# Kernel optimization log

Hardware: AMD Instinct MI355X
Metric: run time of the kernel (lower is better)

The kernel has to match this reference:

```python
import jax, jax.numpy as jnp
import numpy as np

HEADS = 8

def setup_inputs() -> dict:
    key = jax.random.key(0)
    ks = jax.random.split(key, 11)
    B, S, E = 4, 2048, 512
    sc = 1.0 / np.sqrt(E)
    return {
        "inputs": jax.random.normal(ks[0], (B, S, E), jnp.float32),
        "entangle": jax.random.uniform(ks[1], (S,), jnp.float32),
        "Wq": jax.random.normal(ks[2], (E, E), jnp.float32) * sc,
        "bq": jax.random.normal(ks[3], (E,), jnp.float32) * 0.01,
        "Wk": jax.random.normal(ks[4], (E, E), jnp.float32) * sc,
        "bk": jax.random.normal(ks[5], (E,), jnp.float32) * 0.01,
        "Wv": jax.random.normal(ks[6], (E, E), jnp.float32) * sc,
        "bv": jax.random.normal(ks[7], (E,), jnp.float32) * 0.01,
        "Wo": jax.random.normal(ks[8], (E, E), jnp.float32) * sc,
        "bo": jax.random.normal(ks[9], (E,), jnp.float32) * 0.01,
    }

def reference(inputs, entangle, Wq, bq, Wk, bk, Wv, bv, Wo, bo):
    B, S, E = inputs.shape
    H = HEADS
    D = E // H
    # torch nn.Linear: y = x @ W.T + b
    Q = (inputs @ Wq.T + bq).reshape(B, S, H, D)
    K = (inputs @ Wk.T + bk).reshape(B, S, H, D)
    V = (inputs @ Wv.T + bv).reshape(B, S, H, D)
    scores = jnp.einsum('bqhd,bkhd->bhqk', Q, K) / jnp.sqrt(jnp.float32(D))
    # entangle broadcast as (1,1,S,1): per-query-position scaling before softmax
    scores = scores * entangle[None, None, :, None]
    attn = jax.nn.softmax(scores, axis=-1)
    out = jnp.einsum('bhqk,bkhd->bqhd', attn, V).reshape(B, S, E)
    return out @ Wo.T + bo
```

## Files before the change

### kernel.cpp

```cpp
#include <hip/hip_runtime.h>
#include <hip/hip_bf16.h>

#define BB 4
#define SS 2048
#define EE 512
#define HH 8
#define DD 64

typedef __attribute__((ext_vector_type(8))) short bf16x8;
typedef __attribute__((ext_vector_type(4))) float f32x4;
typedef __attribute__((ext_vector_type(4))) unsigned int u32x4;

__device__ __forceinline__ unsigned short f2bf(float f) {
    __hip_bfloat16 h = __float2bfloat16(f);
    return *reinterpret_cast<unsigned short*>(&h);
}

__device__ __forceinline__ unsigned int cvtpk(float lo, float hi) {
    unsigned int r;
    asm("v_cvt_pk_bf16_f32 %0, %1, %2" : "=v"(r) : "v"(lo), "v"(hi));
    return r;
}

__device__ __forceinline__ void pl32(unsigned int& a, unsigned int& b) {
    asm("v_permlane32_swap_b32 %0, %1" : "+v"(a), "+v"(b));
}
__device__ __forceinline__ void pl16(unsigned int& a, unsigned int& b) {
    asm("v_permlane16_swap_b32 %0, %1" : "+v"(a), "+v"(b));
}

__device__ __forceinline__ void gll16(const unsigned short* g, unsigned short* l) {
    __builtin_amdgcn_global_load_lds(
        (const __attribute__((address_space(1))) unsigned int*)g,
        (__attribute__((address_space(3))) unsigned int*)l,
        16, 0, 0);
}

__global__ __launch_bounds__(256)
void cast_all(const float* __restrict__ x,
              const float* __restrict__ wq, const float* __restrict__ wk,
              const float* __restrict__ wv, const float* __restrict__ wo,
              unsigned short* __restrict__ xb,
              unsigned short* __restrict__ wqb, unsigned short* __restrict__ wkb,
              unsigned short* __restrict__ wvb, unsigned short* __restrict__ wob)
{
    const int bid = blockIdx.x;
    const float* src; unsigned short* dst; int lb;
    if (bid < 4096)      { src = x;  dst = xb;  lb = bid; }
    else {
        const int t = (bid - 4096) >> 8;
        lb = (bid - 4096) & 255;
        switch (t) {
            case 0:  src = wq; dst = wqb; break;
            case 1:  src = wk; dst = wkb; break;
            case 2:  src = wv; dst = wvb; break;
            default: src = wo; dst = wob; break;
        }
    }
    const int i = lb * 256 + threadIdx.x;
    const float4 v = reinterpret_cast<const float4*>(src)[i];
    ushort4 o;
    o.x = f2bf(v.x); o.y = f2bf(v.y); o.z = f2bf(v.z); o.w = f2bf(v.w);
    reinterpret_cast<ushort4*>(dst)[i] = o;
}

template<typename OutT, bool TRANSPOSE_V, int TM>
__global__ __launch_bounds__(256)
void gemm_mfma_nt(const unsigned short* __restrict__ A,
                  const unsigned short* __restrict__ W0, const float* __restrict__ b0, OutT* __restrict__ C0,
                  const unsigned short* __restrict__ W1, const float* __restrict__ b1, OutT* __restrict__ C1,
                  const unsigned short* __restrict__ W2, const float* __restrict__ b2, OutT* __restrict__ C2,
                  const float* __restrict__ rowscale,
                  int M, int N, int K)
{
    const unsigned short* W = (blockIdx.z == 0) ? W0 : (blockIdx.z == 1) ? W1 : W2;
    const float* bias       = (blockIdx.z == 0) ? b0 : (blockIdx.z == 1) ? b1 : b2;
    OutT* C                 = (blockIdx.z == 0) ? C0 : (blockIdx.z == 1) ? C1 : C2;

    constexpr int MT = TM / 32;
    __shared__ unsigned short As[2][TM * 32];
    __shared__ unsigned short Bs[2][128 * 32];

    const int tid  = threadIdx.x;
    const int wave = tid >> 6, lane = tid & 63;
    const int quad = lane >> 4, r16 = lane & 15;
    const int m0 = blockIdx.x * TM, n0 = blockIdx.y * 128;
    const int wm0 = (wave >> 1) * (TM / 2), wn0 = (wave & 1) * 64;

    f32x4 acc[MT][4];
    const f32x4 zero = {0.f, 0.f, 0.f, 0.f};
    #pragma unroll
    for (int i = 0; i < MT; ++i)
        #pragma unroll
        for (int j = 0; j < 4; ++j) acc[i][j] = zero;

    const int swz = (r16 >> 1) & 3;

    auto stage = [&](int bi, int k0) {
        #pragma unroll
        for (int j = 0; j < TM / 64; ++j) {
            const int cb = wave * 64 + j * 256;
            const int c  = cb + lane;
            const int row = c >> 2, cc = (c & 3) ^ ((row >> 1) & 3);
            gll16(&A[(size_t)(m0 + row) * K + k0 + cc * 8], &As[bi][cb * 8]);
        }
        #pragma unroll
        for (int j = 0; j < 2; ++j) {
            const int cb = wave * 64 + j * 256;
            const int c  = cb + lane;
            const int row = c >> 2, cc = (c & 3) ^ ((row >> 1) & 3);
            gll16(&W[(size_t)(n0 + row) * K + k0 + cc * 8], &Bs[bi][cb * 8]);
        }
    };

    stage(0, 0);

    const int NI = K / 32;
    for (int i = 0; i < NI; ++i) {
        const int cur = i & 1;
        __syncthreads();
        if (i + 1 < NI) stage(cur ^ 1, (i + 1) * 32);

        bf16x8 af[MT], bfr[4];
        #pragma unroll
        for (int t = 0; t < MT; ++t)
            af[t]  = *reinterpret_cast<bf16x8*>(&As[cur][((wm0 + t * 16 + r16) * 4 + (quad ^ swz)) * 8]);
        #pragma unroll
        for (int t = 0; t < 4; ++t)
            bfr[t] = *reinterpret_cast<bf16x8*>(&Bs[cur][((wn0 + t * 16 + r16) * 4 + (quad ^ swz)) * 8]);
        #pragma unroll
        for (int mt = 0; mt < MT; ++mt)
            #pragma unroll
            for (int nt = 0; nt < 4; ++nt)
                acc[mt][nt] = __builtin_amdgcn_mfma_f32_16x16x32_bf16(
                    af[mt], bfr[nt], acc[mt][nt], 0, 0, 0);
    }

    if (TRANSPOSE_V && blockIdx.z == 2) {
        #pragma unroll
        for (int mt = 0; mt < MT; ++mt) {
            const int m = m0 + wm0 + mt * 16 + quad * 4;
            const int bb = m >> 11, s0 = m & (SS - 1);
            #pragma unroll
            for (int nt = 0; nt < 4; ++nt) {
                const int col = n0 + wn0 + nt * 16 + r16;
                const float bv = bias[col];
                uint2 o;
                o.x = cvtpk(acc[mt][nt][0] + bv, acc[mt][nt][1] + bv);
                o.y = cvtpk(acc[mt][nt][2] + bv, acc[mt][nt][3] + bv);
                *reinterpret_cast<uint2*>(
                    &((unsigned short*)C2)[(size_t)bb * EE * SS + (size_t)col * SS + s0]) = o;
            }
        }
        return;
    }
    const bool doscale = (rowscale != nullptr) && (blockIdx.z == 0);
    #pragma unroll
    for (int mt = 0; mt < MT; ++mt) {
        float rs[4];
        #pragma unroll
        for (int r = 0; r < 4; ++r) {
            const int row = m0 + wm0 + mt * 16 + quad * 4 + r;
            rs[r] = doscale ? rowscale[row & (SS - 1)] * 0.18033688f : 1.0f;
        }
        #pragma unroll
        for (int nt = 0; nt < 4; ++nt) {
            const int col = n0 + wn0 + nt * 16 + r16;
            const float bv = bias[col];
            #pragma unroll
            for (int r = 0; r < 4; ++r) {
                const int row = m0 + wm0 + mt * 16 + quad * 4 + r;
                const float v = (acc[mt][nt][r] + bv) * rs[r];
                if constexpr (sizeof(OutT) == 2)
                    C[(size_t)row * N + col] = (OutT)f2bf(v);
                else
                    C[(size_t)row * N + col] = (OutT)v;
            }
        }
    }
}

__global__ __launch_bounds__(256)
void attn_mfma(const unsigned short* __restrict__ Q,
               const unsigned short* __restrict__ K,
               const unsigned short* __restrict__ Vt,
               unsigned short* __restrict__ O)
{
    __shared__ unsigned short Ks[2][64 * 64];
    __shared__ unsigned short Vs[2][64 * 64];

    const int tid  = threadIdx.x;
    const int wave = tid >> 6, lane = tid & 63;
    const int quad = lane >> 4, r16 = lane & 15;
    const int h  = blockIdx.x;
    const int q0 = blockIdx.y * 64;
    const int b  = blockIdx.z;
    const size_t base    = (size_t)b * SS * EE + (size_t)h * DD;
    const size_t base_vt = ((size_t)b * HH + h) * DD * SS;

    const int qrow = q0 + wave * 16 + r16;
    bf16x8 qf0 = *reinterpret_cast<const bf16x8*>(&Q[base + (size_t)qrow * EE + quad * 8]);
    bf16x8 qf1 = *reinterpret_cast<const bf16x8*>(&Q[base + (size_t)qrow * EE + 32 + quad * 8]);

    const int cb0 = wave * 64, cb1 = wave * 64 + 256;
    const int c0 = cb0 + lane, c1 = cb1 + lane;
    const int row0 = c0 >> 3, cc0 = (c0 & 7) ^ (row0 & 7);
    const int row1 = c1 >> 3, cc1 = (c1 & 7) ^ (row1 & 7);
    const unsigned short* kp0 = &K[base + (size_t)row0 * EE + cc0 * 8];
    const unsigned short* kp1 = &K[base + (size_t)row1 * EE + cc1 * 8];
    const unsigned short* vp0 = &Vt[base_vt + (size_t)row0 * SS + cc0 * 8];
    const unsigned short* vp1 = &Vt[base_vt + (size_t)row1 * SS + cc1 * 8];

    auto stage = [&](int bi, int kt) {
        const size_t ko = (size_t)kt * 64 * EE;
        const int    vo = kt * 64;
        gll16(kp0 + ko, &Ks[bi][cb0 * 8]);
        gll16(vp0 + vo, &Vs[bi][cb0 * 8]);
        gll16(kp1 + ko, &Ks[bi][cb1 * 8]);
        gll16(vp1 + vo, &Vs[bi][cb1 * 8]);
    };

    float l_lane = 0.f;
    f32x4 o_acc[4];
    const f32x4 zero = {0.f, 0.f, 0.f, 0.f};
    #pragma unroll
    for (int dt = 0; dt < 4; ++dt) o_acc[dt] = zero;

    const int swz = r16 & 7;

    stage(0, 0);

    constexpr int NT = SS / 64;
    for (int kt = 0; kt < NT; ++kt) {
        const int cur = kt & 1;
        __syncthreads();
        if (kt + 1 < NT) stage(cur ^ 1, kt + 1);

        f32x4 st[4];
        #pragma unroll
        for (int tn = 0; tn < 4; ++tn) st[tn] = zero;
        #pragma unroll
        for (int tn = 0; tn < 4; ++tn) {
            bf16x8 kf0 = *reinterpret_cast<const bf16x8*>(&Ks[cur][((tn * 16 + r16) * 8 + (quad ^ swz)) * 8]);
            bf16x8 kf1 = *reinterpret_cast<const bf16x8*>(&Ks[cur][((tn * 16 + r16) * 8 + ((quad + 4) ^ swz)) * 8]);
            st[tn] = __builtin_amdgcn_mfma_f32_16x16x32_bf16(kf0, qf0, st[tn], 0, 0, 0);
            st[tn] = __builtin_amdgcn_mfma_f32_16x16x32_bf16(kf1, qf1, st[tn], 0, 0, 0);
        }

        bf16x8 vf0[4], vf1[4];
        #pragma unroll
        for (int dt = 0; dt < 4; ++dt) {
            vf0[dt] = *reinterpret_cast<const bf16x8*>(&Vs[cur][((dt * 16 + r16) * 8 + (quad ^ swz)) * 8]);
            vf1[dt] = *reinterpret_cast<const bf16x8*>(&Vs[cur][((dt * 16 + r16) * 8 + ((quad + 4) ^ swz)) * 8]);
        }

        unsigned int w[4][2];
        #pragma unroll
        for (int tn = 0; tn < 4; ++tn) {
            const float p0 = exp2f(st[tn][0]);
            const float p1 = exp2f(st[tn][1]);
            const float p2 = exp2f(st[tn][2]);
            const float p3 = exp2f(st[tn][3]);
            l_lane += (p0 + p1) + (p2 + p3);
            w[tn][0] = cvtpk(p0, p1);
            w[tn][1] = cvtpk(p2, p3);
        }

        unsigned int pa0 = w[0][0], pa2 = w[1][0];
        pl32(pa0, pa2); pl16(pa0, pa2);
        unsigned int pa1 = w[0][1], pa3 = w[1][1];
        pl32(pa1, pa3); pl16(pa1, pa3);
        unsigned int pb0 = w[2][0], pb2 = w[3][0];
        pl32(pb0, pb2); pl16(pb0, pb2);
        unsigned int pb1 = w[2][1], pb3 = w[3][1];
        pl32(pb1, pb3); pl16(pb1, pb3);

        const u32x4 ua = {pa0, pa1, pa2, pa3};
        const u32x4 ub = {pb0, pb1, pb2, pb3};
        const bf16x8 pf0 = __builtin_bit_cast(bf16x8, ua);
        const bf16x8 pf1 = __builtin_bit_cast(bf16x8, ub);

        #pragma unroll
        for (int dt = 0; dt < 4; ++dt) {
            o_acc[dt] = __builtin_amdgcn_mfma_f32_16x16x32_bf16(pf0, vf0[dt], o_acc[dt], 0, 0, 0);
            o_acc[dt] = __builtin_amdgcn_mfma_f32_16x16x32_bf16(pf1, vf1[dt], o_acc[dt], 0, 0, 0);
        }
    }

    float l = l_lane;
    l += __shfl_xor(l, 16, 64);
    l += __shfl_xor(l, 32, 64);

    #pragma unroll
    for (int r = 0; r < 4; ++r) {
        const float il = 1.0f / __shfl(l, quad * 4 + r, 64);
        const int q = q0 + wave * 16 + quad * 4 + r;
        #pragma unroll
        for (int dt = 0; dt < 4; ++dt)
            O[base + (size_t)q * EE + dt * 16 + r16] = f2bf(o_acc[dt][r] * il);
    }
}

extern "C" void kernel_launch(void* const* d_in, const int* in_sizes, int n_in,
                              void* d_out, int out_size, void* d_ws, size_t ws_size,
                              hipStream_t stream) {
    const float* x   = (const float*)d_in[0];
    const float* ent = (const float*)d_in[1];
    const float* Wq  = (const float*)d_in[2];
    const float* bq  = (const float*)d_in[3];
    const float* Wk  = (const float*)d_in[4];
    const float* bk  = (const float*)d_in[5];
    const float* Wv  = (const float*)d_in[6];
    const float* bv  = (const float*)d_in[7];
    const float* Wo  = (const float*)d_in[8];
    const float* bo  = (const float*)d_in[9];
    float* out = (float*)d_out;

    const size_t n_x = (size_t)BB * SS * EE;
    const size_t n_w = (size_t)EE * EE;

    unsigned short* xb  = (unsigned short*)d_ws;
    unsigned short* wqb = xb + n_x;
    unsigned short* wkb = wqb + n_w;
    unsigned short* wvb = wkb + n_w;
    unsigned short* wob = wvb + n_w;
    unsigned short* Qb  = wob + n_w;
    unsigned short* Kb  = Qb + n_x;
    unsigned short* Vtb = Kb + n_x;
    unsigned short* AOb = Vtb + n_x;

    const int M = BB * SS;

    dim3 gc(4096 + 4 * 256, 1, 1);
    cast_all<<<gc, 256, 0, stream>>>(x, Wq, Wk, Wv, Wo, xb, wqb, wkb, wvb, wob);

    dim3 gq(M / 128, EE / 128, 3);
    gemm_mfma_nt<unsigned short, true, 128><<<gq, 256, 0, stream>>>(
        xb, wqb, bq, Qb, wkb, bk, Kb, wvb, bv, Vtb, ent, M, EE, EE);

    dim3 ga(HH, SS / 64, BB);
    attn_mfma<<<ga, 256, 0, stream>>>(Qb, Kb, Vtb, AOb);

    dim3 go(M / 64, EE / 128, 1);
    gemm_mfma_nt<float, false, 64><<<go, 256, 0, stream>>>(
        AOb, wob, bo, out, wob, bo, out, wob, bo, out, nullptr, M, EE, EE);
}
```

Measured before the change: 187.5 us.

## Process two query sub-tiles per attention block with triple-buffered K/V staging

The attention kernel now handles 128 query rows per block (two 64-row sub-tiles per wave), so each K/V tile staged into LDS is reused for twice as many queries, halving global K/V traffic and the block count. The LDS pipeline moves from double to triple buffering with explicit vmcnt waits and raw barriers so loads run two tiles ahead. In exchange there are more registers per thread, fewer blocks in the grid (512), and more LDS per block, which may reduce occupancy.

Result: slower. 192.8 us (+2.8%).

```diff
diff --git a/kernel.cpp b/kernel.cpp
--- a/kernel.cpp
+++ b/kernel.cpp
@@ -180,27 +180,35 @@
     }
 }
 
+#define QBLK 128
+
 __global__ __launch_bounds__(256)
 void attn_mfma(const unsigned short* __restrict__ Q,
                const unsigned short* __restrict__ K,
                const unsigned short* __restrict__ Vt,
                unsigned short* __restrict__ O)
 {
-    __shared__ unsigned short Ks[2][64 * 64];
-    __shared__ unsigned short Vs[2][64 * 64];
+    __shared__ unsigned short Ks[3][72 * 64];
+    __shared__ unsigned short Vs[3][72 * 64];
 
     const int tid  = threadIdx.x;
     const int wave = tid >> 6, lane = tid & 63;
     const int quad = lane >> 4, r16 = lane & 15;
     const int h  = blockIdx.x;
-    const int q0 = blockIdx.y * 64;
+    const int q0 = blockIdx.y * QBLK;
     const int b  = blockIdx.z;
     const size_t base    = (size_t)b * SS * EE + (size_t)h * DD;
     const size_t base_vt = ((size_t)b * HH + h) * DD * SS;
 
-    const int qrow = q0 + wave * 16 + r16;
-    bf16x8 qf0 = *reinterpret_cast<const bf16x8*>(&Q[base + (size_t)qrow * EE + quad * 8]);
-    bf16x8 qf1 = *reinterpret_cast<const bf16x8*>(&Q[base + (size_t)qrow * EE + 32 + quad * 8]);
+    bf16x8 qf[2][2];
+    #pragma unroll
+    for (int s = 0; s < 2; ++s) {
+        const int qrow = q0 + s * 64 + wave * 16 + r16;
+        #pragma unroll
+        for (int dh = 0; dh < 2; ++dh)
+            qf[s][dh] = *reinterpret_cast<const bf16x8*>(
+                &Q[base + (size_t)qrow * EE + dh * 32 + quad * 8]);
+    }
 
     const int cb0 = wave * 64, cb1 = wave * 64 + 256;
     const int c0 = cb0 + lane, c1 = cb1 + lane;
@@ -220,84 +228,106 @@
         gll16(vp1 + vo, &Vs[bi][cb1 * 8]);
     };
 
-    float l_lane = 0.f;
-    f32x4 o_acc[4];
+    float l_lane[2] = {0.f, 0.f};
+    f32x4 o_acc[2][4];
     const f32x4 zero = {0.f, 0.f, 0.f, 0.f};
     #pragma unroll
-    for (int dt = 0; dt < 4; ++dt) o_acc[dt] = zero;
+    for (int s = 0; s < 2; ++s)
+        #pragma unroll
+        for (int dt = 0; dt < 4; ++dt) o_acc[s][dt] = zero;
 
     const int swz = r16 & 7;
 
     stage(0, 0);
+    stage(1, 1);
 
     constexpr int NT = SS / 64;
     for (int kt = 0; kt < NT; ++kt) {
-        const int cur = kt & 1;
-        __syncthreads();
-        if (kt + 1 < NT) stage(cur ^ 1, kt + 1);
-
-        f32x4 st[4];
-        #pragma unroll
-        for (int tn = 0; tn < 4; ++tn) st[tn] = zero;
+        const int cur = kt % 3;
+        if (kt + 1 < NT) asm volatile("s_waitcnt vmcnt(4)" ::: "memory");
+        else             asm volatile("s_waitcnt vmcnt(0)" ::: "memory");
+        __builtin_amdgcn_s_barrier();
+        __builtin_amdgcn_sched_barrier(0);
+        if (kt + 2 < NT) stage((kt + 2) % 3, kt + 2);
+
+        const unsigned short* Kc = &Ks[cur][0];
+        const unsigned short* Vc = &Vs[cur][0];
+
+        bf16x8 kfA[4], kfB[4];
         #pragma unroll
         for (int tn = 0; tn < 4; ++tn) {
-            bf16x8 kf0 = *reinterpret_cast<const bf16x8*>(&Ks[cur][((tn * 16 + r16) * 8 + (quad ^ swz)) * 8]);
-            bf16x8 kf1 = *reinterpret_cast<const bf16x8*>(&Ks[cur][((tn * 16 + r16) * 8 + ((quad + 4) ^ swz)) * 8]);
-            st[tn] = __builtin_amdgcn_mfma_f32_16x16x32_bf16(kf0, qf0, st[tn], 0, 0, 0);
-            st[tn] = __builtin_amdgcn_mfma_f32_16x16x32_bf16(kf1, qf1, st[tn], 0, 0, 0);
-        }
-
-        bf16x8 vf0[4], vf1[4];
+            kfA[tn] = *reinterpret_cast<const bf16x8*>(&Kc[((tn * 16 + r16) * 8 + (quad ^ swz)) * 8]);
+            kfB[tn] = *reinterpret_cast<const bf16x8*>(&Kc[((tn * 16 + r16) * 8 + ((quad + 4) ^ swz)) * 8]);
+        }
+
+        f32x4 st[2][4];
+        #pragma unroll
+        for (int s = 0; s < 2; ++s)
+            #pragma unroll
+            for (int tn = 0; tn < 4; ++tn) st[s][tn] = zero;
+        #pragma unroll
+        for (int s = 0; s < 2; ++s)
+            #pragma unroll
+            for (int tn = 0; tn < 4; ++tn) {
+                st[s][tn] = __builtin_amdgcn_mfma_f32_16x16x32_bf16(kfA[tn], qf[s][0], st[s][tn], 0, 0, 0);
+                st[s][tn] = __builtin_amdgcn_mfma_f32_16x16x32_bf16(kfB[tn], qf[s][1], st[s][tn], 0, 0, 0);
+            }
+
+        bf16x8 vfA[4], vfB[4];
         #pragma unroll
         for (int dt = 0; dt < 4; ++dt) {
-            vf0[dt] = *reinterpret_cast<const bf16x8*>(&Vs[cur][((dt * 16 + r16) * 8 + (quad ^ swz)) * 8]);
-            vf1[dt] = *reinterpret_cast<const bf16x8*>(&Vs[cur][((dt * 16 + r16) * 8 + ((quad + 4) ^ swz)) * 8]);
-        }
-
-        unsigned int w[4][2];
-        #pragma unroll
-        for (int tn = 0; tn < 4; ++tn) {
-            const float p0 = exp2f(st[tn][0]);
-            const float p1 = exp2f(st[tn][1]);
-            const float p2 = exp2f(st[tn][2]);
-            const float p3 = exp2f(st[tn][3]);
-            l_lane += (p0 + p1) + (p2 + p3);
-            w[tn][0] = cvtpk(p0, p1);
-            w[tn][1] = cvtpk(p2, p3);
-        }
-
-        unsigned int pa0 = w[0][0], pa2 = w[1][0];
-        pl32(pa0, pa2); pl16(pa0, pa2);
-        unsigned int pa1 = w[0][1], pa3 = w[1][1];
-        pl32(pa1, pa3); pl16(pa1, pa3);
-        unsigned int pb0 = w[2][0], pb2 = w[3][0];
-        pl32(pb0, pb2); pl16(pb0, pb2);
-        unsigned int pb1 = w[2][1], pb3 = w[3][1];
-        pl32(pb1, pb3); pl16(pb1, pb3);
-
-        const u32x4 ua = {pa0, pa1, pa2, pa3};
-        const u32x4 ub = {pb0, pb1, pb2, pb3};
-        const bf16x8 pf0 = __builtin_bit_cast(bf16x8, ua);
-        const bf16x8 pf1 = __builtin_bit_cast(bf16x8, ub);
-
-        #pragma unroll
-        for (int dt = 0; dt < 4; ++dt) {
-            o_acc[dt] = __builtin_amdgcn_mfma_f32_16x16x32_bf16(pf0, vf0[dt], o_acc[dt], 0, 0, 0);
-            o_acc[dt] = __builtin_amdgcn_mfma_f32_16x16x32_bf16(pf1, vf1[dt], o_acc[dt], 0, 0, 0);
-        }
-    }
-
-    float l = l_lane;
-    l += __shfl_xor(l, 16, 64);
-    l += __shfl_xor(l, 32, 64);
-
-    #pragma unroll
-    for (int r = 0; r < 4; ++r) {
-        const float il = 1.0f / __shfl(l, quad * 4 + r, 64);
-        const int q = q0 + wave * 16 + quad * 4 + r;
-        #pragma unroll
-        for (int dt = 0; dt < 4; ++dt)
-            O[base + (size_t)q * EE + dt * 16 + r16] = f2bf(o_acc[dt][r] * il);
+            vfA[dt] = *reinterpret_cast<const bf16x8*>(&Vc[((dt * 16 + r16) * 8 + (quad ^ swz)) * 8]);
+            vfB[dt] = *reinterpret_cast<const bf16x8*>(&Vc[((dt * 16 + r16) * 8 + ((quad + 4) ^ swz)) * 8]);
+        }
+
+        #pragma unroll
+        for (int s = 0; s < 2; ++s) {
+            unsigned int w[4][2];
+            #pragma unroll
+            for (int tn = 0; tn < 4; ++tn) {
+                const float p0 = exp2f(st[s][tn][0]);
+                const float p1 = exp2f(st[s][tn][1]);
+                const float p2 = exp2f(st[s][tn][2]);
+                const float p3 = exp2f(st[s][tn][3]);
+                l_lane[s] += (p0 + p1) + (p2 + p3);
+                w[tn][0] = cvtpk(p0, p1);
+                w[tn][1] = cvtpk(p2, p3);
+            }
+            unsigned int pa0 = w[0][0], pa2 = w[1][0];
+            pl32(pa0, pa2); pl16(pa0, pa2);
+            unsigned int pa1 = w[0][1], pa3 = w[1][1];
+            pl32(pa1, pa3); pl16(pa1, pa3);
+            unsigned int pb0 = w[2][0], pb2 = w[3][0];
+            pl32(pb0, pb2); pl16(pb0, pb2);
+            unsigned int pb1 = w[2][1], pb3 = w[3][1];
+            pl32(pb1, pb3); pl16(pb1, pb3);
+
+            const u32x4 ua = {pa0, pa1, pa2, pa3};
+            const u32x4 ub = {pb0, pb1, pb2, pb3};
+            const bf16x8 pf0 = __builtin_bit_cast(bf16x8, ua);
+            const bf16x8 pf1 = __builtin_bit_cast(bf16x8, ub);
+
+            #pragma unroll
+            for (int dt = 0; dt < 4; ++dt) {
+                o_acc[s][dt] = __builtin_amdgcn_mfma_f32_16x16x32_bf16(pf0, vfA[dt], o_acc[s][dt], 0, 0, 0);
+                o_acc[s][dt] = __builtin_amdgcn_mfma_f32_16x16x32_bf16(pf1, vfB[dt], o_acc[s][dt], 0, 0, 0);
+            }
+        }
+    }
+
+    #pragma unroll
+    for (int s = 0; s < 2; ++s) {
+        float l = l_lane[s];
+        l += __shfl_xor(l, 16, 64);
+        l += __shfl_xor(l, 32, 64);
+        #pragma unroll
+        for (int r = 0; r < 4; ++r) {
+            const float il = 1.0f / __shfl(l, quad * 4 + r, 64);
+            const int q = q0 + s * 64 + wave * 16 + quad * 4 + r;
+            #pragma unroll
+            for (int dt = 0; dt < 4; ++dt)
+                O[base + (size_t)q * EE + dt * 16 + r16] = f2bf(o_acc[s][dt][r] * il);
+        }
     }
 }
 
@@ -338,7 +368,7 @@
     gemm_mfma_nt<unsigned short, true, 128><<<gq, 256, 0, stream>>>(
         xb, wqb, bq, Qb, wkb, bk, Kb, wvb, bv, Vtb, ent, M, EE, EE);
 
-    dim3 ga(HH, SS / 64, BB);
+    dim3 ga(HH, SS / QBLK, BB);
     attn_mfma<<<ga, 256, 0, stream>>>(Qb, Kb, Vtb, AOb);
 
     dim3 go(M / 64, EE / 128, 1);
```
